# Kernel tuning notes

Hardware: AMD Instinct MI355X
Metric: run time of the kernel (lower is better)

## Reference

```python
import jax, jax.numpy as jnp
from jax import lax
import numpy as np

B, H, W, C = 512, 64, 128, 3
FEAT = 13 * 26 * 64  # ceil(64/5)*ceil(128/5)*(32+32) after SAME stride-5 convs + concat


def setup_inputs() -> dict:
    key = jax.random.key(0)
    ks = jax.random.split(key, 6)
    x = jax.random.normal(ks[0], (B, H, W, C), jnp.float32)
    conv0_w = jax.random.normal(ks[1], (3, 3, 3, 32), jnp.float32) * 0.05  # HWIO
    conv1_w = jax.random.normal(ks[2], (5, 5, 3, 32), jnp.float32) * 0.05
    fc0_w = jax.random.normal(ks[3], (FEAT, 32), jnp.float32) * 0.01
    fc0_b = jnp.zeros((32,), jnp.float32)
    fc1_w = jax.random.normal(ks[4], (32, 6), jnp.float32) * 0.1
    fc1_b = jnp.zeros((6,), jnp.float32)
    return {"x": x, "conv0_w": conv0_w, "conv1_w": conv1_w,
            "fc0_w": fc0_w, "fc0_b": fc0_b, "fc1_w": fc1_w, "fc1_b": fc1_b}


def _stn_forward(x, conv0_w, conv1_w, fc0_w, fc0_b, fc1_w, fc1_b):
    b, h, w, c = x.shape
    dn = ("NHWC", "HWIO", "NHWC")
    # ---- LocNet ----
    # AveragePooling2D(3x3, stride 1, SAME); TF avg_pool averages over valid
    # (non-padded) elements only, so normalize by a window-count map.
    psum = lax.reduce_window(x, 0.0, lax.add, (1, 3, 3, 1), (1, 1, 1, 1), "SAME")
    cnt = lax.reduce_window(jnp.ones((1, h, w, 1), x.dtype), 0.0, lax.add,
                            (1, 3, 3, 1), (1, 1, 1, 1), "SAME")
    pooled = psum / cnt
    x0 = jax.nn.relu(lax.conv_general_dilated(pooled, conv0_w, (5, 5), "SAME",
                                              dimension_numbers=dn))
    x1 = jax.nn.relu(lax.conv_general_dilated(x, conv1_w, (5, 5), "SAME",
                                              dimension_numbers=dn))
    feat = jnp.concatenate([x0, x1], axis=-1).reshape(b, -1)
    # Dropout(0.5) is identity at inference.
    hid = jnp.tanh(feat @ fc0_w + fc0_b)
    theta = jnp.tanh(hid @ fc1_w + fc1_b).reshape(b, 2, 3)
    # ---- gen_grid ----
    xt, yt = jnp.meshgrid(jnp.linspace(-1.0, 1.0, w), jnp.linspace(-1.0, 1.0, h))
    grid = jnp.stack([xt.ravel(), yt.ravel(), jnp.ones(h * w, x.dtype)])  # [3, h*w]
    T = jnp.einsum("bij,jk->bik", theta, grid)          # [b, 2, h*w]
    T = T.reshape(b, 2, h, w).transpose(0, 2, 3, 1)     # [b, h, w, 2]
    # ---- grid_sample (bilinear) ----
    gx = (T[..., 0] + 1.0) * w / 2.0
    gy = (T[..., 1] + 1.0) * h / 2.0
    x0f = jnp.clip(jnp.floor(gx), 0.0, w - 2.0)
    x1f = jnp.clip(jnp.floor(gx) + 1.0, 1.0, w - 1.0)
    y0f = jnp.clip(jnp.floor(gy), 0.0, h - 2.0)
    y1f = jnp.clip(jnp.floor(gy) + 1.0, 1.0, h - 1.0)
    xi0, xi1 = x0f.astype(jnp.int32), x1f.astype(jnp.int32)
    yi0, yi1 = y0f.astype(jnp.int32), y1f.astype(jnp.int32)
    bi = jnp.arange(b)[:, None, None]                   # broadcast batch index
    Q00 = x[bi, yi0, xi0]  # [b, h, w, c]
    Q01 = x[bi, yi1, xi0]
    Q10 = x[bi, yi0, xi1]
    Q11 = x[bi, yi1, xi1]
    wx0 = (x1f - gx)[..., None]
    wx1 = (gx - x0f)[..., None]
    wy0 = (y1f - gy)[..., None]
    wy1 = (gy - y0f)[..., None]
    # Wx @ Q @ Wy expanded: rows of Q are x-neighbors, cols are y-neighbors.
    out = wx0 * (wy0 * Q00 + wy1 * Q01) + wx1 * (wy0 * Q10 + wy1 * Q11)
    Wd = ((x1f - x0f) * (y1f - y0f))[..., None]
    return out / Wd


def reference(x, conv0_w, conv1_w, fc0_w, fc0_b, fc1_w, fc1_b):
    return _stn_forward(x, conv0_w, conv1_w, fc0_w, fc0_b, fc1_w, fc1_b)
```

## Files before the change

### kernel.cpp

```cpp
#include <hip/hip_runtime.h>
#include <math.h>

namespace {
constexpr int BN = 512, HH = 64, WW = 128, CC = 3;
constexpr int OHH = 13, OWW = 26;
constexpr int NPOS = OHH * OWW;
constexpr int PCH = 26;
constexpr int NPC = NPOS / PCH;
}

__global__ __launch_bounds__(256, 2) void k_locnet(const float* __restrict__ x,
                                                   const float* __restrict__ w0,
                                                   const float* __restrict__ w1,
                                                   const float* __restrict__ fw0,
                                                   float* __restrict__ part) {
  const int pos = blockIdx.x >> 1;
  const int b = ((blockIdx.x & 1) << 8) + threadIdx.x;
  const int oh = pos / 26;
  const int ow = pos - oh * 26;
  const float* xb = x + (size_t)b * (HH * WW * CC);

  const int r0 = oh * 5 - 1;
  const int ri_lo = (oh == 0) ? 1 : 0;
  const int ri_hi = (oh == OHH - 1) ? 4 : 5;
  float xv[6][15];
  if (ow > 0 && ow < OWW - 1) {
    float4 q[6][4];
#pragma unroll
    for (int ri = 0; ri < 6; ++ri) {
      if (ri >= ri_lo && ri <= ri_hi) {
        const float* rp = xb + (size_t)(r0 + ri) * (WW * CC) + (ow * 5 - 1) * 3;
        q[ri][0] = *(const float4*)(rp);
        q[ri][1] = *(const float4*)(rp + 4);
        q[ri][2] = *(const float4*)(rp + 8);
        q[ri][3] = *(const float4*)(rp + 12);
      }
    }
#pragma unroll
    for (int ri = 0; ri < 6; ++ri) {
      if (ri < ri_lo || ri > ri_hi) {
#pragma unroll
        for (int c = 0; c < 15; ++c) xv[ri][c] = 0.f;
      } else {
        xv[ri][0] = q[ri][0].x; xv[ri][1] = q[ri][0].y; xv[ri][2] = q[ri][0].z;
        xv[ri][3] = q[ri][0].w; xv[ri][4] = q[ri][1].x; xv[ri][5] = q[ri][1].y;
        xv[ri][6] = q[ri][1].z; xv[ri][7] = q[ri][1].w; xv[ri][8] = q[ri][2].x;
        xv[ri][9] = q[ri][2].y; xv[ri][10] = q[ri][2].z; xv[ri][11] = q[ri][2].w;
        xv[ri][12] = q[ri][3].x; xv[ri][13] = q[ri][3].y; xv[ri][14] = q[ri][3].z;
      }
    }
  } else {
#pragma unroll
    for (int ri = 0; ri < 6; ++ri) {
      const int gr = r0 + ri;
      const int grc = min(max(gr, 0), HH - 1);
      const bool rv = (gr >= 0) & (gr <= HH - 1);
      const float* rowp = xb + grc * (WW * CC);
#pragma unroll
      for (int pj = 0; pj < 5; ++pj) {
        const int gc = ow * 5 - 1 + pj;
        const int gcc = min(max(gc, 0), WW - 1);
        const bool v = rv & (gc >= 0) & (gc <= WW - 1);
        const float* pp = rowp + gcc * CC;
        const float f0 = pp[0], f1 = pp[1], f2 = pp[2];
        xv[ri][pj * 3 + 0] = v ? f0 : 0.f;
        xv[ri][pj * 3 + 1] = v ? f1 : 0.f;
        xv[ri][pj * 3 + 2] = v ? f2 : 0.f;
      }
    }
  }

  float hacc[32];
#pragma unroll
  for (int n = 0; n < 32; ++n) hacc[n] = 0.f;

#pragma unroll 1
  for (int qg = 0; qg < 8; ++qg) {
    float a0 = 0.f, a1 = 0.f, a2 = 0.f, a3 = 0.f;
#pragma unroll
    for (int kh = 0; kh < 5; ++kh)
#pragma unroll
      for (int kw = 0; kw < 5; ++kw)
#pragma unroll
        for (int ic = 0; ic < 3; ++ic) {
          const float pv = xv[kh + 1][kw * 3 + ic];
          const int tap = (kh * 5 + kw) * 3 + ic;
          const float4 wv = *(const float4*)(w1 + tap * 32 + qg * 4);
          a0 += pv * wv.x; a1 += pv * wv.y; a2 += pv * wv.z; a3 += pv * wv.w;
        }
    const float a[4] = {fmaxf(a0, 0.f), fmaxf(a1, 0.f),
                        fmaxf(a2, 0.f), fmaxf(a3, 0.f)};
    const float* wr = fw0 + ((size_t)pos * 64 + 32 + qg * 4) * 32;
#pragma unroll
    for (int j = 0; j < 4; ++j) {
      const float aj = a[j];
#pragma unroll
      for (int q2 = 0; q2 < 8; ++q2) {
        const float4 wv = *(const float4*)(wr + j * 32 + q2 * 4);
        hacc[q2 * 4 + 0] += aj * wv.x; hacc[q2 * 4 + 1] += aj * wv.y;
        hacc[q2 * 4 + 2] += aj * wv.z; hacc[q2 * 4 + 3] += aj * wv.w;
      }
    }
  }

  float inv[3][3];
#pragma unroll
  for (int kh = 0; kh < 3; ++kh)
#pragma unroll
    for (int kw = 0; kw < 3; ++kw) {
      const int rc = 3 - ((oh == 0 && kh == 0) ? 1 : 0);
      int cc2 = 3;
      if (ow == 0 && kw == 0) cc2 = 2;
      if (ow == OWW - 1 && kw == 2) cc2 = 2;
      inv[kh][kw] = 1.0f / (float)(rc * cc2);
    }
  float pooled[27];
#pragma unroll
  for (int kh = 0; kh < 3; ++kh)
#pragma unroll
    for (int kw = 0; kw < 3; ++kw)
#pragma unroll
      for (int ic = 0; ic < 3; ++ic) {
        float s = 0.f;
#pragma unroll
        for (int dr = 0; dr < 3; ++dr)
#pragma unroll
          for (int dc = 0; dc < 3; ++dc)
            s += xv[kh + dr][(kw + dc) * 3 + ic];
        pooled[(kh * 3 + kw) * 3 + ic] = s * inv[kh][kw];
      }

#pragma unroll 1
  for (int qg = 0; qg < 8; ++qg) {
    float a0 = 0.f, a1 = 0.f, a2 = 0.f, a3 = 0.f;
#pragma unroll
    for (int tap = 0; tap < 27; ++tap) {
      const float pv = pooled[tap];
      const float4 wv = *(const float4*)(w0 + tap * 32 + qg * 4);
      a0 += pv * wv.x; a1 += pv * wv.y; a2 += pv * wv.z; a3 += pv * wv.w;
    }
    const float a[4] = {fmaxf(a0, 0.f), fmaxf(a1, 0.f),
                        fmaxf(a2, 0.f), fmaxf(a3, 0.f)};
    const float* wr = fw0 + ((size_t)pos * 64 + qg * 4) * 32;
#pragma unroll
    for (int j = 0; j < 4; ++j) {
      const float aj = a[j];
#pragma unroll
      for (int q2 = 0; q2 < 8; ++q2) {
        const float4 wv = *(const float4*)(wr + j * 32 + q2 * 4);
        hacc[q2 * 4 + 0] += aj * wv.x; hacc[q2 * 4 + 1] += aj * wv.y;
        hacc[q2 * 4 + 2] += aj * wv.z; hacc[q2 * 4 + 3] += aj * wv.w;
      }
    }
  }

  float* po = part + (size_t)pos * 32 * 512 + b;
#pragma unroll
  for (int n = 0; n < 32; ++n) po[(size_t)n * 512] = hacc[n];
}

__global__ __launch_bounds__(256) void k_theta1(const float* __restrict__ part,
                                                float* __restrict__ part2) {
  const int pc = blockIdx.x >> 3;
  const int bc = blockIdx.x & 7;
  const int lane = threadIdx.x & 63;
  const int og = threadIdx.x >> 6;
  const int bcol = bc * 64 + lane;
  float acc[8] = {0.f, 0.f, 0.f, 0.f, 0.f, 0.f, 0.f, 0.f};
  const float* pp = part + ((size_t)pc * PCH * 32 + og * 8) * 512 + bcol;
  for (int pq = 0; pq < PCH; ++pq) {
#pragma unroll
    for (int j = 0; j < 8; ++j)
      acc[j] += pp[((size_t)pq * 32 + j) * 512];
  }
  float* o = part2 + ((size_t)pc * 32 + og * 8) * 512 + bcol;
#pragma unroll
  for (int j = 0; j < 8; ++j) o[(size_t)j * 512] = acc[j];
}

__global__ __launch_bounds__(256) void k_theta2(const float* __restrict__ part2,
                                                const float* __restrict__ b0,
                                                const float* __restrict__ w1f,
                                                const float* __restrict__ b1,
                                                float* __restrict__ theta) {
  __shared__ float hid[64][32];
  const int lane = threadIdx.x & 63;
  const int og = threadIdx.x >> 6;
  const int bcol = blockIdx.x * 64 + lane;
#pragma unroll
  for (int j = 0; j < 8; ++j) {
    const int oc = og * 8 + j;
    float s = b0[oc];
#pragma unroll
    for (int pc = 0; pc < NPC; ++pc)
      s += part2[((size_t)pc * 32 + oc) * 512 + bcol];
    hid[lane][oc] = tanhf(s);
  }
  __syncthreads();
  for (int u = threadIdx.x; u < 64 * 6; u += 256) {
    const int bl = u / 6, j = u - bl * 6;
    float s2 = b1[j];
#pragma unroll
    for (int oc = 0; oc < 32; ++oc) s2 += hid[bl][oc] * w1f[oc * 6 + j];
    theta[(blockIdx.x * 64 + bl) * 6 + j] = tanhf(s2);
  }
}

__global__ __launch_bounds__(256) void k_sample(const float* __restrict__ x,
                                                const float* __restrict__ theta,
                                                float* __restrict__ out) {
  const int b = blockIdx.x >> 3;
  const int seg = blockIdx.x & 7;
  __shared__ float th[6];
  if (threadIdx.x < 6) th[threadIdx.x] = theta[b * 6 + threadIdx.x];
  __syncthreads();
  const float t00 = th[0], t01 = th[1], t02 = th[2];
  const float t10 = th[3], t11 = th[4], t12 = th[5];
  const int idx = seg * 1024 + threadIdx.x * 4;
  const int i = idx >> 7, j0 = idx & 127;
  const float yt = (float)i * (2.0f / 63.0f) - 1.0f;
  const float* xb = x + (size_t)b * (HH * WW * CC);
  float res[12];
#pragma unroll
  for (int p = 0; p < 4; ++p) {
    const float xt = (float)(j0 + p) * (2.0f / 127.0f) - 1.0f;
    const float gx = (t00 * xt + t01 * yt + t02 + 1.0f) * 64.0f;
    const float gy = (t10 * xt + t11 * yt + t12 + 1.0f) * 32.0f;
    const float fx = floorf(gx), fy = floorf(gy);
    const float x0f = fminf(fmaxf(fx, 0.f), 126.f);
    const float x1f = fminf(fmaxf(fx + 1.f, 1.f), 127.f);
    const float y0f = fminf(fmaxf(fy, 0.f), 62.f);
    const float y1f = fminf(fmaxf(fy + 1.f, 1.f), 63.f);
    const float wx0 = x1f - gx, wx1 = gx - x0f;
    const float wy0 = y1f - gy, wy1 = gy - y0f;
    const int xi0 = (int)x0f, xi1 = (int)x1f;
    const int yi0 = (int)y0f, yi1 = (int)y1f;
    const float* q00 = xb + (yi0 * WW + xi0) * 3;
    const float* q01 = xb + (yi1 * WW + xi0) * 3;
    const float* q10 = xb + (yi0 * WW + xi1) * 3;
    const float* q11 = xb + (yi1 * WW + xi1) * 3;
#pragma unroll
    for (int c = 0; c < 3; ++c)
      res[p * 3 + c] = wx0 * (wy0 * q00[c] + wy1 * q01[c]) +
                       wx1 * (wy0 * q10[c] + wy1 * q11[c]);
  }
  float4* o = (float4*)(out + ((size_t)b * 8192 + idx) * 3);
  o[0] = make_float4(res[0], res[1], res[2], res[3]);
  o[1] = make_float4(res[4], res[5], res[6], res[7]);
  o[2] = make_float4(res[8], res[9], res[10], res[11]);
}

extern "C" void kernel_launch(void* const* d_in, const int* in_sizes, int n_in,
                              void* d_out, int out_size, void* d_ws, size_t ws_size,
                              hipStream_t stream) {
  (void)in_sizes; (void)n_in; (void)out_size; (void)ws_size;
  const float* x   = (const float*)d_in[0];
  const float* w0  = (const float*)d_in[1];
  const float* w1  = (const float*)d_in[2];
  const float* fw0 = (const float*)d_in[3];
  const float* fb0 = (const float*)d_in[4];
  const float* fw1 = (const float*)d_in[5];
  const float* fb1 = (const float*)d_in[6];
  float* outp = (float*)d_out;
  float* part  = outp;
  float* part2 = outp + (size_t)NPOS * 32 * 512;
  float* theta = (float*)d_ws;
  k_locnet<<<NPOS * 2, 256, 0, stream>>>(x, w0, w1, fw0, part);
  k_theta1<<<NPC * 8, 256, 0, stream>>>(part, part2);
  k_theta2<<<8, 256, 0, stream>>>(part2, fb0, fw1, fb1, theta);
  k_sample<<<BN * 8, 256, 0, stream>>>(x, theta, outp);
}
```

Baseline: 138.8 us.

## Split locnet threads into pool/conv0 and conv1 roles with XCD-aware block mapping

Each locnet block now uses 128 samples with two thread roles. One half computes avg-pool plus conv0, the other computes conv1, and each writes its own partial slab of the fc0 projection. This doubles the grid, halves per-thread work and register footprint, and remaps block indices so consecutive positions spread across XCDs. The cost is twice the partial-sum traffic that k_theta1 must write and then reduce.

```diff
diff --git a/kernel.cpp b/kernel.cpp
--- a/kernel.cpp
+++ b/kernel.cpp
@@ -5,31 +5,34 @@
 constexpr int BN = 512, HH = 64, WW = 128, CC = 3;
 constexpr int OHH = 13, OWW = 26;
 constexpr int NPOS = OHH * OWW;
+constexpr int NSLAB = NPOS * 2;
 constexpr int PCH = 26;
-constexpr int NPC = NPOS / PCH;
-}
-
-__global__ __launch_bounds__(256, 2) void k_locnet(const float* __restrict__ x,
-                                                   const float* __restrict__ w0,
-                                                   const float* __restrict__ w1,
-                                                   const float* __restrict__ fw0,
-                                                   float* __restrict__ part) {
-  const int pos = blockIdx.x >> 1;
-  const int b = ((blockIdx.x & 1) << 8) + threadIdx.x;
-  const int oh = pos / 26;
-  const int ow = pos - oh * 26;
+constexpr int NPC = NSLAB / PCH;
+}
+
+__global__ __launch_bounds__(256) void k_locnet(const float* __restrict__ x,
+                                                const float* __restrict__ w0,
+                                                const float* __restrict__ w1,
+                                                const float* __restrict__ fw0,
+                                                float* __restrict__ part) {
+  const int cpx = (NPOS * 4) >> 3;
+  const int L = (blockIdx.x & 7) * cpx + (blockIdx.x >> 3);
+  const int bc = L / NPOS;
+  const int pos = L - bc * NPOS;
+  const int oh = pos / OWW, ow = pos - oh * OWW;
+  const int role = threadIdx.x >> 7;
+  const int b = bc * 128 + (threadIdx.x & 127);
   const float* xb = x + (size_t)b * (HH * WW * CC);
 
-  const int r0 = oh * 5 - 1;
-  const int ri_lo = (oh == 0) ? 1 : 0;
-  const int ri_hi = (oh == OHH - 1) ? 4 : 5;
-  float xv[6][15];
+  const int rbase = oh * 5 - 1 + role;
+  float xv[5][15];
   if (ow > 0 && ow < OWW - 1) {
-    float4 q[6][4];
-#pragma unroll
-    for (int ri = 0; ri < 6; ++ri) {
-      if (ri >= ri_lo && ri <= ri_hi) {
-        const float* rp = xb + (size_t)(r0 + ri) * (WW * CC) + (ow * 5 - 1) * 3;
+    float4 q[5][4];
+#pragma unroll
+    for (int ri = 0; ri < 5; ++ri) {
+      const int gr = rbase + ri;
+      if (gr >= 0 && gr < HH) {
+        const float* rp = xb + (size_t)gr * (WW * CC) + (ow * 5 - 1) * 3;
         q[ri][0] = *(const float4*)(rp);
         q[ri][1] = *(const float4*)(rp + 4);
         q[ri][2] = *(const float4*)(rp + 8);
@@ -37,8 +40,9 @@
       }
     }
 #pragma unroll
-    for (int ri = 0; ri < 6; ++ri) {
-      if (ri < ri_lo || ri > ri_hi) {
+    for (int ri = 0; ri < 5; ++ri) {
+      const int gr = rbase + ri;
+      if (gr < 0 || gr >= HH) {
 #pragma unroll
         for (int c = 0; c < 15; ++c) xv[ri][c] = 0.f;
       } else {
@@ -51,21 +55,21 @@
     }
   } else {
 #pragma unroll
-    for (int ri = 0; ri < 6; ++ri) {
-      const int gr = r0 + ri;
+    for (int ri = 0; ri < 5; ++ri) {
+      const int gr = rbase + ri;
       const int grc = min(max(gr, 0), HH - 1);
-      const bool rv = (gr >= 0) & (gr <= HH - 1);
+      const bool rv = (gr >= 0) & (gr < HH);
       const float* rowp = xb + grc * (WW * CC);
 #pragma unroll
-      for (int pj = 0; pj < 5; ++pj) {
-        const int gc = ow * 5 - 1 + pj;
+      for (int c = 0; c < 5; ++c) {
+        const int gc = ow * 5 - 1 + c;
         const int gcc = min(max(gc, 0), WW - 1);
-        const bool v = rv & (gc >= 0) & (gc <= WW - 1);
+        const bool v = rv & (gc >= 0) & (gc < WW);
         const float* pp = rowp + gcc * CC;
         const float f0 = pp[0], f1 = pp[1], f2 = pp[2];
-        xv[ri][pj * 3 + 0] = v ? f0 : 0.f;
-        xv[ri][pj * 3 + 1] = v ? f1 : 0.f;
-        xv[ri][pj * 3 + 2] = v ? f2 : 0.f;
+        xv[ri][c * 3 + 0] = v ? f0 : 0.f;
+        xv[ri][c * 3 + 1] = v ? f1 : 0.f;
+        xv[ri][c * 3 + 2] = v ? f2 : 0.f;
       }
     }
   }
@@ -74,87 +78,82 @@
 #pragma unroll
   for (int n = 0; n < 32; ++n) hacc[n] = 0.f;
 
+  if (role == 0) {
+    float pooled[27];
+#pragma unroll
+    for (int kh = 0; kh < 3; ++kh)
+#pragma unroll
+      for (int kw = 0; kw < 3; ++kw) {
+        const int gr = oh * 5 + kh, gc = ow * 5 + kw;
+        const int rc = min(gr + 1, HH - 1) - max(gr - 1, 0) + 1;
+        const int c2 = min(gc + 1, WW - 1) - max(gc - 1, 0) + 1;
+        const float inv = 1.0f / (float)(rc * c2);
+#pragma unroll
+        for (int ic = 0; ic < 3; ++ic) {
+          float s = 0.f;
+#pragma unroll
+          for (int dr = 0; dr < 3; ++dr)
+#pragma unroll
+            for (int dc = 0; dc < 3; ++dc)
+              s += xv[kh + dr][(kw + dc) * 3 + ic];
+          pooled[(kh * 3 + kw) * 3 + ic] = s * inv;
+        }
+      }
 #pragma unroll 1
-  for (int qg = 0; qg < 8; ++qg) {
-    float a0 = 0.f, a1 = 0.f, a2 = 0.f, a3 = 0.f;
-#pragma unroll
-    for (int kh = 0; kh < 5; ++kh)
-#pragma unroll
-      for (int kw = 0; kw < 5; ++kw)
-#pragma unroll
-        for (int ic = 0; ic < 3; ++ic) {
-          const float pv = xv[kh + 1][kw * 3 + ic];
-          const int tap = (kh * 5 + kw) * 3 + ic;
-          const float4 wv = *(const float4*)(w1 + tap * 32 + qg * 4);
-          a0 += pv * wv.x; a1 += pv * wv.y; a2 += pv * wv.z; a3 += pv * wv.w;
+    for (int qg = 0; qg < 8; ++qg) {
+      float a0 = 0.f, a1 = 0.f, a2 = 0.f, a3 = 0.f;
+#pragma unroll
+      for (int tap = 0; tap < 27; ++tap) {
+        const float pv = pooled[tap];
+        const float4 wv = *(const float4*)(w0 + tap * 32 + qg * 4);
+        a0 += pv * wv.x; a1 += pv * wv.y; a2 += pv * wv.z; a3 += pv * wv.w;
+      }
+      const float a[4] = {fmaxf(a0, 0.f), fmaxf(a1, 0.f),
+                          fmaxf(a2, 0.f), fmaxf(a3, 0.f)};
+      const float* wr = fw0 + ((size_t)pos * 64 + qg * 4) * 32;
+#pragma unroll
+      for (int j = 0; j < 4; ++j) {
+        const float aj = a[j];
+#pragma unroll
+        for (int q2 = 0; q2 < 8; ++q2) {
+          const float4 wv = *(const float4*)(wr + j * 32 + q2 * 4);
+          hacc[q2 * 4 + 0] += aj * wv.x; hacc[q2 * 4 + 1] += aj * wv.y;
+          hacc[q2 * 4 + 2] += aj * wv.z; hacc[q2 * 4 + 3] += aj * wv.w;
         }
-    const float a[4] = {fmaxf(a0, 0.f), fmaxf(a1, 0.f),
-                        fmaxf(a2, 0.f), fmaxf(a3, 0.f)};
-    const float* wr = fw0 + ((size_t)pos * 64 + 32 + qg * 4) * 32;
-#pragma unroll
-    for (int j = 0; j < 4; ++j) {
-      const float aj = a[j];
-#pragma unroll
-      for (int q2 = 0; q2 < 8; ++q2) {
-        const float4 wv = *(const float4*)(wr + j * 32 + q2 * 4);
-        hacc[q2 * 4 + 0] += aj * wv.x; hacc[q2 * 4 + 1] += aj * wv.y;
-        hacc[q2 * 4 + 2] += aj * wv.z; hacc[q2 * 4 + 3] += aj * wv.w;
-      }
-    }
-  }
-
-  float inv[3][3];
-#pragma unroll
-  for (int kh = 0; kh < 3; ++kh)
-#pragma unroll
-    for (int kw = 0; kw < 3; ++kw) {
-      const int rc = 3 - ((oh == 0 && kh == 0) ? 1 : 0);
-      int cc2 = 3;
-      if (ow == 0 && kw == 0) cc2 = 2;
-      if (ow == OWW - 1 && kw == 2) cc2 = 2;
-      inv[kh][kw] = 1.0f / (float)(rc * cc2);
-    }
-  float pooled[27];
-#pragma unroll
-  for (int kh = 0; kh < 3; ++kh)
-#pragma unroll
-    for (int kw = 0; kw < 3; ++kw)
-#pragma unroll
-      for (int ic = 0; ic < 3; ++ic) {
-        float s = 0.f;
-#pragma unroll
-        for (int dr = 0; dr < 3; ++dr)
-#pragma unroll
-          for (int dc = 0; dc < 3; ++dc)
-            s += xv[kh + dr][(kw + dc) * 3 + ic];
-        pooled[(kh * 3 + kw) * 3 + ic] = s * inv[kh][kw];
-      }
-
+      }
+    }
+  } else {
 #pragma unroll 1
-  for (int qg = 0; qg < 8; ++qg) {
-    float a0 = 0.f, a1 = 0.f, a2 = 0.f, a3 = 0.f;
-#pragma unroll
-    for (int tap = 0; tap < 27; ++tap) {
-      const float pv = pooled[tap];
-      const float4 wv = *(const float4*)(w0 + tap * 32 + qg * 4);
-      a0 += pv * wv.x; a1 += pv * wv.y; a2 += pv * wv.z; a3 += pv * wv.w;
-    }
-    const float a[4] = {fmaxf(a0, 0.f), fmaxf(a1, 0.f),
-                        fmaxf(a2, 0.f), fmaxf(a3, 0.f)};
-    const float* wr = fw0 + ((size_t)pos * 64 + qg * 4) * 32;
-#pragma unroll
-    for (int j = 0; j < 4; ++j) {
-      const float aj = a[j];
-#pragma unroll
-      for (int q2 = 0; q2 < 8; ++q2) {
-        const float4 wv = *(const float4*)(wr + j * 32 + q2 * 4);
-        hacc[q2 * 4 + 0] += aj * wv.x; hacc[q2 * 4 + 1] += aj * wv.y;
-        hacc[q2 * 4 + 2] += aj * wv.z; hacc[q2 * 4 + 3] += aj * wv.w;
-      }
-    }
-  }
-
-  float* po = part + (size_t)pos * 32 * 512 + b;
+    for (int qg = 0; qg < 8; ++qg) {
+      float a0 = 0.f, a1 = 0.f, a2 = 0.f, a3 = 0.f;
+#pragma unroll
+      for (int kh = 0; kh < 5; ++kh)
+#pragma unroll
+        for (int kw = 0; kw < 5; ++kw)
+#pragma unroll
+          for (int ic = 0; ic < 3; ++ic) {
+            const float pv = xv[kh][kw * 3 + ic];
+            const int tap = (kh * 5 + kw) * 3 + ic;
+            const float4 wv = *(const float4*)(w1 + tap * 32 + qg * 4);
+            a0 += pv * wv.x; a1 += pv * wv.y; a2 += pv * wv.z; a3 += pv * wv.w;
+          }
+      const float a[4] = {fmaxf(a0, 0.f), fmaxf(a1, 0.f),
+                          fmaxf(a2, 0.f), fmaxf(a3, 0.f)};
+      const float* wr = fw0 + ((size_t)pos * 64 + 32 + qg * 4) * 32;
+#pragma unroll
+      for (int j = 0; j < 4; ++j) {
+        const float aj = a[j];
+#pragma unroll
+        for (int q2 = 0; q2 < 8; ++q2) {
+          const float4 wv = *(const float4*)(wr + j * 32 + q2 * 4);
+          hacc[q2 * 4 + 0] += aj * wv.x; hacc[q2 * 4 + 1] += aj * wv.y;
+          hacc[q2 * 4 + 2] += aj * wv.z; hacc[q2 * 4 + 3] += aj * wv.w;
+        }
+      }
+    }
+  }
+
+  float* po = part + (size_t)(pos * 2 + role) * 32 * 512 + b;
 #pragma unroll
   for (int n = 0; n < 32; ++n) po[(size_t)n * 512] = hacc[n];
 }
@@ -162,10 +161,10 @@
 __global__ __launch_bounds__(256) void k_theta1(const float* __restrict__ part,
                                                 float* __restrict__ part2) {
   const int pc = blockIdx.x >> 3;
-  const int bc = blockIdx.x & 7;
+  const int bcs = blockIdx.x & 7;
   const int lane = threadIdx.x & 63;
   const int og = threadIdx.x >> 6;
-  const int bcol = bc * 64 + lane;
+  const int bcol = bcs * 64 + lane;
   float acc[8] = {0.f, 0.f, 0.f, 0.f, 0.f, 0.f, 0.f, 0.f};
   const float* pp = part + ((size_t)pc * PCH * 32 + og * 8) * 512 + bcol;
   for (int pq = 0; pq < PCH; ++pq) {
@@ -263,9 +262,9 @@
   const float* fb1 = (const float*)d_in[6];
   float* outp = (float*)d_out;
   float* part  = outp;
-  float* part2 = outp + (size_t)NPOS * 32 * 512;
+  float* part2 = outp + (size_t)NSLAB * 32 * 512;
   float* theta = (float*)d_ws;
-  k_locnet<<<NPOS * 2, 256, 0, stream>>>(x, w0, w1, fw0, part);
+  k_locnet<<<NPOS * 4, 256, 0, stream>>>(x, w0, w1, fw0, part);
   k_theta1<<<NPC * 8, 256, 0, stream>>>(part, part2);
   k_theta2<<<8, 256, 0, stream>>>(part2, fb0, fw1, fb1, theta);
   k_sample<<<BN * 8, 256, 0, stream>>>(x, theta, outp);
```

Measured after the change: 136.8 us. No clear change (-1.4%).
